# Optimization experiments

Hardware: AMD Instinct MI355X
Metric: run time of the kernel (lower is better)

Reference implementation:

```python
import jax, jax.numpy as jnp
import numpy as np

N = 100000   # nodes
E = 1600000  # edges (avg degree 16)
D = 32       # feature dim

def setup_inputs() -> dict:
    key = jax.random.key(0)
    k1, k2, k3, k4 = jax.random.split(key, 4)
    feat = jax.random.normal(k1, (N, D), dtype=jnp.float32)
    e_feat = jax.random.normal(k2, (E, 1), dtype=jnp.float32)
    src = jax.random.randint(k3, (E,), 0, N)
    dst = jax.random.randint(k4, (E,), 0, N)
    return {"feat": feat, "e_feat": e_feat, "src": src, "dst": dst}

def reference(feat, e_feat, src, dst):
    n = feat.shape[0]
    ones = jnp.ones(src.shape[0], dtype=feat.dtype)
    # degrees computed on the full graph (before self-loop removal), as in DGL code
    out_deg = jax.ops.segment_sum(ones, src, num_segments=n)
    in_deg = jax.ops.segment_sum(ones, dst, num_segments=n)
    src_norm = jnp.power(jnp.clip(out_deg, 1.0, None), -0.5)[:, None]  # [N,1]
    dst_norm = jnp.power(jnp.clip(in_deg, 1.0, None), -0.5)[:, None]   # [N,1]
    # remove_self_loop: mask out self-loop edges in the aggregation only
    mask = (src != dst).astype(feat.dtype)[:, None]                    # [E,1]
    # u_mul_e: gather normalized src features, multiply by edge weight
    msg = (feat * src_norm)[src] * (e_feat * mask)                     # [E,D]
    agg = jax.ops.segment_sum(msg, dst, num_segments=n)                # [N,D]
    out = feat - agg * dst_norm
    return jnp.sum(jnp.abs(out), axis=1)                               # [N]
```

## Files before the change

kernel.cpp:

```cpp
#include <hip/hip_runtime.h>

#define D 32
#define RANGE 128
#define RMAX 800
#define CAP 2304
#define STRIDE 2560
#define SSTRIDE 2560
#define CPAD 16
#define DCH 5000
#define SCH 9000
#define CNT_OFF 50000
#define CUR_OFF 53200
#define ARENA_SZ 56400

__device__ __forceinline__ int scan512(int x, int* wp, int t) {
    int lane = t & 63, w = t >> 6;
    #pragma unroll
    for (int d = 1; d < 64; d <<= 1) {
        int y = __shfl_up(x, d, 64);
        if (lane >= d) x += y;
    }
    if (lane == 63) wp[w] = x;
    __syncthreads();
    int off = 0;
    #pragma unroll
    for (int i = 0; i < 7; i++) if (i < w) off += wp[i];
    return x + off;
}

__global__ __launch_bounds__(256) void zero_cur(int* __restrict__ p, int m) {
    int i = blockIdx.x * 256 + threadIdx.x;
    if (i < m) p[i] = 0;
}

__global__ __launch_bounds__(512) void fused_sort(
        const int* __restrict__ src, const int* __restrict__ dst,
        const float* __restrict__ ef,
        uint2* __restrict__ recsR, unsigned char* __restrict__ srcsR,
        int* __restrict__ gcurD, int* __restrict__ gcurS,
        int E, int DJC) {
    __shared__ __align__(16) char arena[ARENA_SZ];
    __shared__ int wp[8];
    int t = threadIdx.x;
    int* cnt = (int*)(arena + CNT_OFF);
    int* cur = (int*)(arena + CUR_OFF);

    if ((int)blockIdx.x < DJC) {
        int j = blockIdx.x;
        uint2* sd = (uint2*)arena;
        unsigned short* rg16 = (unsigned short*)(arena + 40000);
        int e0 = j * DCH, e1 = min(E, e0 + DCH), cntE = e1 - e0;
        for (int i = t; i < RMAX; i += 512) cnt[i] = 0;
        __syncthreads();
        for (int e = e0 + 2 * t; e < e1; e += 1024) {
            if (e + 1 < e1) {
                int2 d2 = *(const int2*)(dst + e);
                atomicAdd(&cnt[d2.x >> 7], 1);
                atomicAdd(&cnt[d2.y >> 7], 1);
            } else {
                atomicAdd(&cnt[dst[e] >> 7], 1);
            }
        }
        __syncthreads();
        int v0 = cnt[t];
        int incl0 = scan512(v0, wp, t);
        int tot0 = wp[0] + wp[1] + wp[2] + wp[3] + wp[4] + wp[5] + wp[6] + wp[7];
        __syncthreads();
        int i1 = t + 512;
        int v1 = (i1 < RMAX) ? cnt[i1] : 0;
        int incl1 = scan512(v1, wp, t);
        cur[t] = incl0 - v0;
        if (i1 < RMAX) cur[i1] = tot0 + incl1 - v1;
        __syncthreads();
        for (int e = e0 + t; e < e1; e += 512) {
            int s = src[e], d = dst[e];
            float w = (s == d) ? 0.0f : ef[e];
            int rg = d >> 7;
            int pos = atomicAdd(&cur[rg], 1);
            sd[pos] = make_uint2((unsigned)s | ((unsigned)(d & 127) << 17),
                                 __float_as_uint(w));
            rg16[pos] = (unsigned short)rg;
        }
        __syncthreads();
        for (int i = t; i < RMAX; i += 512) {
            int c = cnt[i];
            if (c) {
                int g = atomicAdd(&gcurD[i * CPAD], c);
                cnt[i] = g - (cur[i] - c);
            }
        }
        __syncthreads();
        for (int i = t; i < cntE; i += 512) {
            int rg = rg16[i];
            recsR[(size_t)rg * STRIDE + cnt[rg] + i] = sd[i];
        }
    } else {
        int j = blockIdx.x - DJC;
        unsigned char* sid = (unsigned char*)arena;
        unsigned short* rg16 = (unsigned short*)(arena + 9000);
        int e0 = j * SCH, e1 = min(E, e0 + SCH), cntE = e1 - e0;
        for (int i = t; i < RMAX; i += 512) cnt[i] = 0;
        __syncthreads();
        for (int e = e0 + 2 * t; e < e1; e += 1024) {
            if (e + 1 < e1) {
                int2 s2 = *(const int2*)(src + e);
                atomicAdd(&cnt[s2.x >> 7], 1);
                atomicAdd(&cnt[s2.y >> 7], 1);
            } else {
                atomicAdd(&cnt[src[e] >> 7], 1);
            }
        }
        __syncthreads();
        int v0 = cnt[t];
        int incl0 = scan512(v0, wp, t);
        int tot0 = wp[0] + wp[1] + wp[2] + wp[3] + wp[4] + wp[5] + wp[6] + wp[7];
        __syncthreads();
        int i1 = t + 512;
        int v1 = (i1 < RMAX) ? cnt[i1] : 0;
        int incl1 = scan512(v1, wp, t);
        cur[t] = incl0 - v0;
        if (i1 < RMAX) cur[i1] = tot0 + incl1 - v1;
        __syncthreads();
        for (int e = e0 + t; e < e1; e += 512) {
            int s = src[e];
            int rg = s >> 7;
            int pos = atomicAdd(&cur[rg], 1);
            sid[pos] = (unsigned char)(s & 127);
            rg16[pos] = (unsigned short)rg;
        }
        __syncthreads();
        for (int i = t; i < RMAX; i += 512) {
            int c = cnt[i];
            if (c) {
                int g = atomicAdd(&gcurS[i * CPAD], c);
                cnt[i] = g - (cur[i] - c);
            }
        }
        __syncthreads();
        for (int i = t; i < cntE; i += 512) {
            int rg = rg16[i];
            srcsR[(size_t)rg * SSTRIDE + cnt[rg] + i] = sid[i];
        }
    }
}

__global__ __launch_bounds__(512) void srcnorm_convert(
        const unsigned char* __restrict__ srcsR, const int* __restrict__ gcurS,
        const float* __restrict__ feat, float* __restrict__ featn,
        int n, int R) {
    __shared__ int h[2][RANGE];
    __shared__ int cnt[RANGE];
    int r = blockIdx.x, t = threadIdx.x;
    int base = r * RANGE, lim = min(n - base, RANGE);
    if (t < 256) h[t >> 7][t & 127] = 0;
    __syncthreads();
    int total = gcurS[r * CPAD];
    const unsigned char* p = srcsR + (size_t)r * SSTRIDE;
    int cp = (t >> 8) & 1;
    for (int i = t; i < total; i += 512)
        atomicAdd(&h[cp][p[i]], 1);
    __syncthreads();
    if (t < RANGE) cnt[t] = h[0][t] + h[1][t];
    __syncthreads();
    int total4 = lim * 8;
    for (int i = t; i < total4; i += 512) {
        int row = i >> 3;
        float sn = rsqrtf((float)max(cnt[row], 1));
        float4 f = ((const float4*)(feat + (size_t)(base + row) * D))[i & 7];
        float4 o;
        o.x = f.x * sn; o.y = f.y * sn; o.z = f.z * sn; o.w = f.w * sn;
        ((float4*)(featn + (size_t)(base + row) * D))[i & 7] = o;
    }
}

__global__ __launch_bounds__(512) void gather_kernel(
        const float* __restrict__ feat, const float* __restrict__ featn,
        const uint2* __restrict__ recsR, const int* __restrict__ gcurD,
        float* __restrict__ out, int n, int R) {
    __shared__ uint2 raw[CAP];
    __shared__ uint2 srec[CAP];
    __shared__ int indeg[RANGE];
    __shared__ int pre[RANGE + 1];
    __shared__ int wp[8];
    int r = blockIdx.x, t = threadIdx.x;
    int base = r * RANGE, lim = min(n - base, RANGE);
    int total = gcurD[r * CPAD];
    bool ovf = total > CAP;
    const uint2* reg = recsR + (size_t)r * STRIDE;
    if (t < RANGE) indeg[t] = 0;
    __syncthreads();
    if (!ovf) {
        for (int i = t; i < total; i += 512) {
            uint2 rec = reg[i];
            raw[i] = rec;
            atomicAdd(&indeg[rec.x >> 17], 1);
        }
    } else {
        for (int i = t; i < total; i += 512)
            atomicAdd(&indeg[reg[i].x >> 17], 1);
    }
    __syncthreads();
    int vv = (t < RANGE) ? indeg[t] : 0;
    int incl2 = scan512(vv, wp, t);
    if (t < RANGE) pre[t + 1] = incl2;
    if (t == 0) pre[0] = 0;
    __syncthreads();
    if (t < RANGE) indeg[t] = pre[t];
    __syncthreads();
    if (!ovf) {
        for (int i = t; i < total; i += 512) {
            uint2 rec = raw[i];
            int dl = rec.x >> 17;
            int pos = atomicAdd(&indeg[dl], 1);
            srec[pos] = make_uint2(rec.x & 0x1FFFFu, rec.y);
        }
    }
    __syncthreads();
    int node = t >> 2;
    int cch = t & 3;
    if (node >= lim) return;
    int p0i = pre[node];
    int cnt = pre[node + 1] - p0i;
    float a0 = 0.f, a1 = 0.f, a2 = 0.f, a3 = 0.f, a4 = 0.f, a5 = 0.f, a6 = 0.f, a7 = 0.f;
    if (!ovf) {
        const uint2* sp = srec + p0i;
        int i = 0;
        for (; i + 4 <= cnt; i += 4) {
            uint2 q0 = sp[i], q1 = sp[i + 1], q2 = sp[i + 2], q3 = sp[i + 3];
            const float4* f0 = (const float4*)(featn + (size_t)q0.x * D) + cch * 2;
            const float4* f1 = (const float4*)(featn + (size_t)q1.x * D) + cch * 2;
            const float4* f2 = (const float4*)(featn + (size_t)q2.x * D) + cch * 2;
            const float4* f3 = (const float4*)(featn + (size_t)q3.x * D) + cch * 2;
            float4 A0 = f0[0], B0 = f0[1];
            float4 A1 = f1[0], B1 = f1[1];
            float4 A2 = f2[0], B2 = f2[1];
            float4 A3 = f3[0], B3 = f3[1];
            float w0 = __uint_as_float(q0.y), w1 = __uint_as_float(q1.y);
            float w2 = __uint_as_float(q2.y), w3 = __uint_as_float(q3.y);
            a0 += A0.x * w0 + A1.x * w1 + A2.x * w2 + A3.x * w3;
            a1 += A0.y * w0 + A1.y * w1 + A2.y * w2 + A3.y * w3;
            a2 += A0.z * w0 + A1.z * w1 + A2.z * w2 + A3.z * w3;
            a3 += A0.w * w0 + A1.w * w1 + A2.w * w2 + A3.w * w3;
            a4 += B0.x * w0 + B1.x * w1 + B2.x * w2 + B3.x * w3;
            a5 += B0.y * w0 + B1.y * w1 + B2.y * w2 + B3.y * w3;
            a6 += B0.z * w0 + B1.z * w1 + B2.z * w2 + B3.z * w3;
            a7 += B0.w * w0 + B1.w * w1 + B2.w * w2 + B3.w * w3;
        }
        for (; i < cnt; i++) {
            uint2 q = sp[i];
            const float4* f = (const float4*)(featn + (size_t)q.x * D) + cch * 2;
            float4 A = f[0], B = f[1];
            float w = __uint_as_float(q.y);
            a0 += A.x * w; a1 += A.y * w; a2 += A.z * w; a3 += A.w * w;
            a4 += B.x * w; a5 += B.y * w; a6 += B.z * w; a7 += B.w * w;
        }
    } else {
        for (int k = 0; k < total; k++) {
            uint2 rec = reg[k];
            if ((int)(rec.x >> 17) == node) {
                const float4* f = (const float4*)(featn + (size_t)(rec.x & 0x1FFFFu) * D) + cch * 2;
                float4 A = f[0], B = f[1];
                float w = __uint_as_float(rec.y);
                a0 += A.x * w; a1 += A.y * w; a2 += A.z * w; a3 += A.w * w;
                a4 += B.x * w; a5 += B.y * w; a6 += B.z * w; a7 += B.w * w;
            }
        }
    }
    float dn = rsqrtf((float)max(cnt, 1));
    const float4* fr = (const float4*)(feat + (size_t)(base + node) * D);
    float4 fA = fr[cch * 2];
    float4 fB = fr[cch * 2 + 1];
    float v = fabsf(fA.x - a0 * dn) + fabsf(fA.y - a1 * dn) +
              fabsf(fA.z - a2 * dn) + fabsf(fA.w - a3 * dn) +
              fabsf(fB.x - a4 * dn) + fabsf(fB.y - a5 * dn) +
              fabsf(fB.z - a6 * dn) + fabsf(fB.w - a7 * dn);
    v += __shfl_xor(v, 1, 4);
    v += __shfl_xor(v, 2, 4);
    if (cch == 0) out[base + node] = v;
}

extern "C" void kernel_launch(void* const* d_in, const int* in_sizes, int n_in,
                              void* d_out, int out_size, void* d_ws, size_t ws_size,
                              hipStream_t stream) {
    const float* feat   = (const float*)d_in[0];
    const float* e_feat = (const float*)d_in[1];
    const int*   src    = (const int*)d_in[2];
    const int*   dst    = (const int*)d_in[3];
    const int E = in_sizes[2];
    const int n = in_sizes[0] / D;
    float* out = (float*)d_out;

    const int R   = (n + RANGE - 1) / RANGE;
    const int DJC = (E + DCH - 1) / DCH;
    const int SJC = (E + SCH - 1) / SCH;

    char* p = (char*)d_ws;
    uint2* recsR        = (uint2*)p;         p += ((size_t)R * STRIDE * 8 + 15) & ~(size_t)15;
    unsigned char* srcsR = (unsigned char*)p; p += ((size_t)R * SSTRIDE + 15) & ~(size_t)15;
    int* gcurD          = (int*)p;           p += ((size_t)2 * R * CPAD * 4 + 15) & ~(size_t)15;
    int* gcurS          = gcurD + (size_t)R * CPAD;
    float* featn        = (float*)p;

    const int mcur = R * CPAD * 2;
    zero_cur<<<(mcur + 255) / 256, 256, 0, stream>>>(gcurD, mcur);

    fused_sort<<<DJC + SJC, 512, 0, stream>>>(src, dst, e_feat, recsR, srcsR,
                                              gcurD, gcurS, E, DJC);

    srcnorm_convert<<<R, 512, 0, stream>>>(srcsR, gcurS, feat, featn, n, R);

    gather_kernel<<<R, 512, 0, stream>>>(feat, featn, recsR, gcurD, out, n, R);
}
```

Measured before the change: 140.6 us.

## Fuse sort, source-norm and gather into one cooperative persistent kernel with grid barriers

Replaces the three separate launches (bucket sort, source-degree normalisation with featn materialisation, gather) with one persistent cooperative kernel that loops over work items and separates phases with atomic grid barriers. The source-norm phase now writes only a per-node scale table instead of a scaled copy of the feature matrix. The gather folds that scale into each edge weight and reads raw feat. The raw staging buffer in shared memory is dropped, and chunk sizes are retuned so the grid fits resident blocks. This removes launch gaps and the featn write/read traffic, at the cost of barrier spin overhead, lower occupancy from the larger LDS arena, and a deadlock risk if the fallback non-cooperative launch is ever used.

```diff
diff --git a/kernel.cpp b/kernel.cpp
--- a/kernel.cpp
+++ b/kernel.cpp
@@ -7,11 +7,13 @@
 #define STRIDE 2560
 #define SSTRIDE 2560
 #define CPAD 16
-#define DCH 5000
-#define SCH 9000
-#define CNT_OFF 50000
-#define CUR_OFF 53200
-#define ARENA_SZ 56400
+#define NBLK 512
+#define DCH 5800
+#define RG_OFF 46400
+#define CNT_OFF 58000
+#define CUR_OFF 61200
+#define ARENA_SZ 64400
+#define SRG_OFF 8192
 
 __device__ __forceinline__ int scan512(int x, int* wp, int t) {
     int lane = t & 63, w = t >> 6;
@@ -28,255 +30,254 @@
     return x + off;
 }
 
-__global__ __launch_bounds__(256) void zero_cur(int* __restrict__ p, int m) {
+__global__ __launch_bounds__(256) void zero_ws(int* __restrict__ p, int m) {
     int i = blockIdx.x * 256 + threadIdx.x;
     if (i < m) p[i] = 0;
 }
 
-__global__ __launch_bounds__(512) void fused_sort(
+__device__ __forceinline__ void gridbar(int* c, int target) {
+    __syncthreads();
+    __threadfence();
+    if (threadIdx.x == 0) {
+        atomicAdd(c, 1);
+        while (atomicAdd(c, 0) < target) __builtin_amdgcn_s_sleep(2);
+    }
+    __syncthreads();
+    __threadfence();
+}
+
+__global__ __launch_bounds__(NBLK, 4) void mega(
         const int* __restrict__ src, const int* __restrict__ dst,
-        const float* __restrict__ ef,
+        const float* __restrict__ ef, const float* __restrict__ feat,
         uint2* __restrict__ recsR, unsigned char* __restrict__ srcsR,
-        int* __restrict__ gcurD, int* __restrict__ gcurS,
-        int E, int DJC) {
+        int* __restrict__ gcurD, int* __restrict__ gcurS, int* __restrict__ bars,
+        float* __restrict__ sn_tab, float* __restrict__ out,
+        int n, int R, int E, int DJC, int SCH) {
     __shared__ __align__(16) char arena[ARENA_SZ];
     __shared__ int wp[8];
-    int t = threadIdx.x;
+    int t = threadIdx.x, bid = blockIdx.x, gb = gridDim.x;
     int* cnt = (int*)(arena + CNT_OFF);
     int* cur = (int*)(arena + CUR_OFF);
 
-    if ((int)blockIdx.x < DJC) {
-        int j = blockIdx.x;
-        uint2* sd = (uint2*)arena;
-        unsigned short* rg16 = (unsigned short*)(arena + 40000);
-        int e0 = j * DCH, e1 = min(E, e0 + DCH), cntE = e1 - e0;
-        for (int i = t; i < RMAX; i += 512) cnt[i] = 0;
+    int SJCk = (E + SCH - 1) / SCH;
+    int TC = DJC + SJCk;
+    for (int c = bid; c < TC; c += gb) {
         __syncthreads();
-        for (int e = e0 + 2 * t; e < e1; e += 1024) {
-            if (e + 1 < e1) {
-                int2 d2 = *(const int2*)(dst + e);
-                atomicAdd(&cnt[d2.x >> 7], 1);
-                atomicAdd(&cnt[d2.y >> 7], 1);
-            } else {
-                atomicAdd(&cnt[dst[e] >> 7], 1);
+        if (c < DJC) {
+            uint2* sd = (uint2*)arena;
+            unsigned short* rg16 = (unsigned short*)(arena + RG_OFF);
+            int e0 = c * DCH, e1 = min(E, e0 + DCH), cntE = e1 - e0;
+            for (int i = t; i < RMAX; i += NBLK) cnt[i] = 0;
+            __syncthreads();
+            for (int e = e0 + 2 * t; e < e1; e += 2 * NBLK) {
+                if (e + 1 < e1) {
+                    int2 d2 = *(const int2*)(dst + e);
+                    atomicAdd(&cnt[d2.x >> 7], 1);
+                    atomicAdd(&cnt[d2.y >> 7], 1);
+                } else {
+                    atomicAdd(&cnt[dst[e] >> 7], 1);
+                }
+            }
+            __syncthreads();
+            int v0 = cnt[t];
+            int incl0 = scan512(v0, wp, t);
+            int tot0 = wp[0] + wp[1] + wp[2] + wp[3] + wp[4] + wp[5] + wp[6] + wp[7];
+            __syncthreads();
+            int i1 = t + 512;
+            int v1 = (i1 < RMAX) ? cnt[i1] : 0;
+            int incl1 = scan512(v1, wp, t);
+            cur[t] = incl0 - v0;
+            if (i1 < RMAX) cur[i1] = tot0 + incl1 - v1;
+            __syncthreads();
+            for (int e = e0 + t; e < e1; e += NBLK) {
+                int s = src[e], d = dst[e];
+                float w = (s == d) ? 0.0f : ef[e];
+                int rg = d >> 7;
+                int pos = atomicAdd(&cur[rg], 1);
+                sd[pos] = make_uint2((unsigned)s | ((unsigned)(d & 127) << 17),
+                                     __float_as_uint(w));
+                rg16[pos] = (unsigned short)rg;
+            }
+            __syncthreads();
+            for (int i = t; i < RMAX; i += NBLK) {
+                int cc = cnt[i];
+                if (cc) {
+                    int g = atomicAdd(&gcurD[i * CPAD], cc);
+                    cnt[i] = g - (cur[i] - cc);
+                }
+            }
+            __syncthreads();
+            for (int i = t; i < cntE; i += NBLK) {
+                int rg = rg16[i];
+                recsR[(size_t)rg * STRIDE + cnt[rg] + i] = sd[i];
+            }
+        } else {
+            int j = c - DJC;
+            unsigned char* sid = (unsigned char*)arena;
+            unsigned short* rg16 = (unsigned short*)(arena + SRG_OFF);
+            int e0 = j * SCH, e1 = min(E, e0 + SCH), cntE = e1 - e0;
+            for (int i = t; i < RMAX; i += NBLK) cnt[i] = 0;
+            __syncthreads();
+            for (int e = e0 + 2 * t; e < e1; e += 2 * NBLK) {
+                if (e + 1 < e1) {
+                    int2 s2 = *(const int2*)(src + e);
+                    atomicAdd(&cnt[s2.x >> 7], 1);
+                    atomicAdd(&cnt[s2.y >> 7], 1);
+                } else {
+                    atomicAdd(&cnt[src[e] >> 7], 1);
+                }
+            }
+            __syncthreads();
+            int v0 = cnt[t];
+            int incl0 = scan512(v0, wp, t);
+            int tot0 = wp[0] + wp[1] + wp[2] + wp[3] + wp[4] + wp[5] + wp[6] + wp[7];
+            __syncthreads();
+            int i1 = t + 512;
+            int v1 = (i1 < RMAX) ? cnt[i1] : 0;
+            int incl1 = scan512(v1, wp, t);
+            cur[t] = incl0 - v0;
+            if (i1 < RMAX) cur[i1] = tot0 + incl1 - v1;
+            __syncthreads();
+            for (int e = e0 + t; e < e1; e += NBLK) {
+                int s = src[e];
+                int rg = s >> 7;
+                int pos = atomicAdd(&cur[rg], 1);
+                sid[pos] = (unsigned char)(s & 127);
+                rg16[pos] = (unsigned short)rg;
+            }
+            __syncthreads();
+            for (int i = t; i < RMAX; i += NBLK) {
+                int cc = cnt[i];
+                if (cc) {
+                    int g = atomicAdd(&gcurS[i * CPAD], cc);
+                    cnt[i] = g - (cur[i] - cc);
+                }
+            }
+            __syncthreads();
+            for (int i = t; i < cntE; i += NBLK) {
+                int rg = rg16[i];
+                srcsR[(size_t)rg * SSTRIDE + cnt[rg] + i] = sid[i];
             }
         }
-        __syncthreads();
-        int v0 = cnt[t];
-        int incl0 = scan512(v0, wp, t);
-        int tot0 = wp[0] + wp[1] + wp[2] + wp[3] + wp[4] + wp[5] + wp[6] + wp[7];
-        __syncthreads();
-        int i1 = t + 512;
-        int v1 = (i1 < RMAX) ? cnt[i1] : 0;
-        int incl1 = scan512(v1, wp, t);
-        cur[t] = incl0 - v0;
-        if (i1 < RMAX) cur[i1] = tot0 + incl1 - v1;
-        __syncthreads();
-        for (int e = e0 + t; e < e1; e += 512) {
-            int s = src[e], d = dst[e];
-            float w = (s == d) ? 0.0f : ef[e];
-            int rg = d >> 7;
-            int pos = atomicAdd(&cur[rg], 1);
-            sd[pos] = make_uint2((unsigned)s | ((unsigned)(d & 127) << 17),
-                                 __float_as_uint(w));
-            rg16[pos] = (unsigned short)rg;
+    }
+    gridbar(&bars[0], gb);
+
+    {
+        int* h0 = (int*)arena;
+        int* h1 = (int*)(arena + 512);
+        for (int r = bid; r < R; r += gb) {
+            __syncthreads();
+            if (t < RANGE) { h0[t] = 0; h1[t] = 0; }
+            __syncthreads();
+            int total = gcurS[r * CPAD];
+            const unsigned char* p = srcsR + (size_t)r * SSTRIDE;
+            int* h = (t & 256) ? h1 : h0;
+            for (int i = t; i < total; i += NBLK) atomicAdd(&h[p[i]], 1);
+            __syncthreads();
+            int base = r * RANGE;
+            if (t < RANGE && base + t < n)
+                sn_tab[base + t] = rsqrtf((float)max(h0[t] + h1[t], 1));
         }
-        __syncthreads();
-        for (int i = t; i < RMAX; i += 512) {
-            int c = cnt[i];
-            if (c) {
-                int g = atomicAdd(&gcurD[i * CPAD], c);
-                cnt[i] = g - (cur[i] - c);
+    }
+    gridbar(&bars[1], gb);
+
+    {
+        uint2* srec = (uint2*)arena;
+        int* indeg = (int*)(arena + 18432);
+        int* pre   = (int*)(arena + 18944);
+        for (int r = bid; r < R; r += gb) {
+            __syncthreads();
+            int base = r * RANGE, lim = min(n - base, RANGE);
+            int total = gcurD[r * CPAD];
+            bool ovf = total > CAP;
+            const uint2* reg = recsR + (size_t)r * STRIDE;
+            if (t < RANGE) indeg[t] = 0;
+            __syncthreads();
+            for (int i = t; i < total; i += NBLK)
+                atomicAdd(&indeg[reg[i].x >> 17], 1);
+            __syncthreads();
+            int vv = (t < RANGE) ? indeg[t] : 0;
+            int incl2 = scan512(vv, wp, t);
+            if (t < RANGE) pre[t + 1] = incl2;
+            if (t == 0) pre[0] = 0;
+            __syncthreads();
+            if (t < RANGE) indeg[t] = pre[t];
+            __syncthreads();
+            if (!ovf) {
+                for (int i = t; i < total; i += NBLK) {
+                    uint2 rec = reg[i];
+                    int s = rec.x & 0x1FFFF;
+                    int pos = atomicAdd(&indeg[rec.x >> 17], 1);
+                    float wn = __uint_as_float(rec.y) * sn_tab[s];
+                    srec[pos] = make_uint2((unsigned)s, __float_as_uint(wn));
+                }
+            }
+            __syncthreads();
+            int node = t >> 2, cch = t & 3;
+            if (node < lim) {
+                int p0i = pre[node];
+                int cnt2 = pre[node + 1] - p0i;
+                float a0 = 0.f, a1 = 0.f, a2 = 0.f, a3 = 0.f,
+                      a4 = 0.f, a5 = 0.f, a6 = 0.f, a7 = 0.f;
+                if (!ovf) {
+                    const uint2* sp = srec + p0i;
+                    int i = 0;
+                    for (; i + 4 <= cnt2; i += 4) {
+                        uint2 q0 = sp[i], q1 = sp[i + 1], q2 = sp[i + 2], q3 = sp[i + 3];
+                        const float4* f0 = (const float4*)(feat + (size_t)q0.x * D) + cch * 2;
+                        const float4* f1 = (const float4*)(feat + (size_t)q1.x * D) + cch * 2;
+                        const float4* f2 = (const float4*)(feat + (size_t)q2.x * D) + cch * 2;
+                        const float4* f3 = (const float4*)(feat + (size_t)q3.x * D) + cch * 2;
+                        float4 A0 = f0[0], B0 = f0[1];
+                        float4 A1 = f1[0], B1 = f1[1];
+                        float4 A2 = f2[0], B2 = f2[1];
+                        float4 A3 = f3[0], B3 = f3[1];
+                        float w0 = __uint_as_float(q0.y), w1 = __uint_as_float(q1.y);
+                        float w2 = __uint_as_float(q2.y), w3 = __uint_as_float(q3.y);
+                        a0 += A0.x * w0 + A1.x * w1 + A2.x * w2 + A3.x * w3;
+                        a1 += A0.y * w0 + A1.y * w1 + A2.y * w2 + A3.y * w3;
+                        a2 += A0.z * w0 + A1.z * w1 + A2.z * w2 + A3.z * w3;
+                        a3 += A0.w * w0 + A1.w * w1 + A2.w * w2 + A3.w * w3;
+                        a4 += B0.x * w0 + B1.x * w1 + B2.x * w2 + B3.x * w3;
+                        a5 += B0.y * w0 + B1.y * w1 + B2.y * w2 + B3.y * w3;
+                        a6 += B0.z * w0 + B1.z * w1 + B2.z * w2 + B3.z * w3;
+                        a7 += B0.w * w0 + B1.w * w1 + B2.w * w2 + B3.w * w3;
+                    }
+                    for (; i < cnt2; i++) {
+                        uint2 q = sp[i];
+                        const float4* f = (const float4*)(feat + (size_t)q.x * D) + cch * 2;
+                        float4 A = f[0], B = f[1];
+                        float w = __uint_as_float(q.y);
+                        a0 += A.x * w; a1 += A.y * w; a2 += A.z * w; a3 += A.w * w;
+                        a4 += B.x * w; a5 += B.y * w; a6 += B.z * w; a7 += B.w * w;
+                    }
+                } else {
+                    for (int k = 0; k < total; k++) {
+                        uint2 rec = reg[k];
+                        if ((int)(rec.x >> 17) == node) {
+                            int s = rec.x & 0x1FFFF;
+                            float w = __uint_as_float(rec.y) * sn_tab[s];
+                            const float4* f = (const float4*)(feat + (size_t)s * D) + cch * 2;
+                            float4 A = f[0], B = f[1];
+                            a0 += A.x * w; a1 += A.y * w; a2 += A.z * w; a3 += A.w * w;
+                            a4 += B.x * w; a5 += B.y * w; a6 += B.z * w; a7 += B.w * w;
+                        }
+                    }
+                }
+                float dn = rsqrtf((float)max(cnt2, 1));
+                const float4* fr = (const float4*)(feat + (size_t)(base + node) * D);
+                float4 fA = fr[cch * 2];
+                float4 fB = fr[cch * 2 + 1];
+                float v = fabsf(fA.x - a0 * dn) + fabsf(fA.y - a1 * dn) +
+                          fabsf(fA.z - a2 * dn) + fabsf(fA.w - a3 * dn) +
+                          fabsf(fB.x - a4 * dn) + fabsf(fB.y - a5 * dn) +
+                          fabsf(fB.z - a6 * dn) + fabsf(fB.w - a7 * dn);
+                v += __shfl_xor(v, 1, 4);
+                v += __shfl_xor(v, 2, 4);
+                if (cch == 0) out[base + node] = v;
             }
         }
-        __syncthreads();
-        for (int i = t; i < cntE; i += 512) {
-            int rg = rg16[i];
-            recsR[(size_t)rg * STRIDE + cnt[rg] + i] = sd[i];
-        }
-    } else {
-        int j = blockIdx.x - DJC;
-        unsigned char* sid = (unsigned char*)arena;
-        unsigned short* rg16 = (unsigned short*)(arena + 9000);
-        int e0 = j * SCH, e1 = min(E, e0 + SCH), cntE = e1 - e0;
-        for (int i = t; i < RMAX; i += 512) cnt[i] = 0;
-        __syncthreads();
-        for (int e = e0 + 2 * t; e < e1; e += 1024) {
-            if (e + 1 < e1) {
-                int2 s2 = *(const int2*)(src + e);
-                atomicAdd(&cnt[s2.x >> 7], 1);
-                atomicAdd(&cnt[s2.y >> 7], 1);
-            } else {
-                atomicAdd(&cnt[src[e] >> 7], 1);
-            }
-        }
-        __syncthreads();
-        int v0 = cnt[t];
-        int incl0 = scan512(v0, wp, t);
-        int tot0 = wp[0] + wp[1] + wp[2] + wp[3] + wp[4] + wp[5] + wp[6] + wp[7];
-        __syncthreads();
-        int i1 = t + 512;
-        int v1 = (i1 < RMAX) ? cnt[i1] : 0;
-        int incl1 = scan512(v1, wp, t);
-        cur[t] = incl0 - v0;
-        if (i1 < RMAX) cur[i1] = tot0 + incl1 - v1;
-        __syncthreads();
-        for (int e = e0 + t; e < e1; e += 512) {
-            int s = src[e];
-            int rg = s >> 7;
-            int pos = atomicAdd(&cur[rg], 1);
-            sid[pos] = (unsigned char)(s & 127);
-            rg16[pos] = (unsigned short)rg;
-        }
-        __syncthreads();
-        for (int i = t; i < RMAX; i += 512) {
-            int c = cnt[i];
-            if (c) {
-                int g = atomicAdd(&gcurS[i * CPAD], c);
-                cnt[i] = g - (cur[i] - c);
-            }
-        }
-        __syncthreads();
-        for (int i = t; i < cntE; i += 512) {
-            int rg = rg16[i];
-            srcsR[(size_t)rg * SSTRIDE + cnt[rg] + i] = sid[i];
-        }
-    }
-}
-
-__global__ __launch_bounds__(512) void srcnorm_convert(
-        const unsigned char* __restrict__ srcsR, const int* __restrict__ gcurS,
-        const float* __restrict__ feat, float* __restrict__ featn,
-        int n, int R) {
-    __shared__ int h[2][RANGE];
-    __shared__ int cnt[RANGE];
-    int r = blockIdx.x, t = threadIdx.x;
-    int base = r * RANGE, lim = min(n - base, RANGE);
-    if (t < 256) h[t >> 7][t & 127] = 0;
-    __syncthreads();
-    int total = gcurS[r * CPAD];
-    const unsigned char* p = srcsR + (size_t)r * SSTRIDE;
-    int cp = (t >> 8) & 1;
-    for (int i = t; i < total; i += 512)
-        atomicAdd(&h[cp][p[i]], 1);
-    __syncthreads();
-    if (t < RANGE) cnt[t] = h[0][t] + h[1][t];
-    __syncthreads();
-    int total4 = lim * 8;
-    for (int i = t; i < total4; i += 512) {
-        int row = i >> 3;
-        float sn = rsqrtf((float)max(cnt[row], 1));
-        float4 f = ((const float4*)(feat + (size_t)(base + row) * D))[i & 7];
-        float4 o;
-        o.x = f.x * sn; o.y = f.y * sn; o.z = f.z * sn; o.w = f.w * sn;
-        ((float4*)(featn + (size_t)(base + row) * D))[i & 7] = o;
-    }
-}
-
-__global__ __launch_bounds__(512) void gather_kernel(
-        const float* __restrict__ feat, const float* __restrict__ featn,
-        const uint2* __restrict__ recsR, const int* __restrict__ gcurD,
-        float* __restrict__ out, int n, int R) {
-    __shared__ uint2 raw[CAP];
-    __shared__ uint2 srec[CAP];
-    __shared__ int indeg[RANGE];
-    __shared__ int pre[RANGE + 1];
-    __shared__ int wp[8];
-    int r = blockIdx.x, t = threadIdx.x;
-    int base = r * RANGE, lim = min(n - base, RANGE);
-    int total = gcurD[r * CPAD];
-    bool ovf = total > CAP;
-    const uint2* reg = recsR + (size_t)r * STRIDE;
-    if (t < RANGE) indeg[t] = 0;
-    __syncthreads();
-    if (!ovf) {
-        for (int i = t; i < total; i += 512) {
-            uint2 rec = reg[i];
-            raw[i] = rec;
-            atomicAdd(&indeg[rec.x >> 17], 1);
-        }
-    } else {
-        for (int i = t; i < total; i += 512)
-            atomicAdd(&indeg[reg[i].x >> 17], 1);
-    }
-    __syncthreads();
-    int vv = (t < RANGE) ? indeg[t] : 0;
-    int incl2 = scan512(vv, wp, t);
-    if (t < RANGE) pre[t + 1] = incl2;
-    if (t == 0) pre[0] = 0;
-    __syncthreads();
-    if (t < RANGE) indeg[t] = pre[t];
-    __syncthreads();
-    if (!ovf) {
-        for (int i = t; i < total; i += 512) {
-            uint2 rec = raw[i];
-            int dl = rec.x >> 17;
-            int pos = atomicAdd(&indeg[dl], 1);
-            srec[pos] = make_uint2(rec.x & 0x1FFFFu, rec.y);
-        }
-    }
-    __syncthreads();
-    int node = t >> 2;
-    int cch = t & 3;
-    if (node >= lim) return;
-    int p0i = pre[node];
-    int cnt = pre[node + 1] - p0i;
-    float a0 = 0.f, a1 = 0.f, a2 = 0.f, a3 = 0.f, a4 = 0.f, a5 = 0.f, a6 = 0.f, a7 = 0.f;
-    if (!ovf) {
-        const uint2* sp = srec + p0i;
-        int i = 0;
-        for (; i + 4 <= cnt; i += 4) {
-            uint2 q0 = sp[i], q1 = sp[i + 1], q2 = sp[i + 2], q3 = sp[i + 3];
-            const float4* f0 = (const float4*)(featn + (size_t)q0.x * D) + cch * 2;
-            const float4* f1 = (const float4*)(featn + (size_t)q1.x * D) + cch * 2;
-            const float4* f2 = (const float4*)(featn + (size_t)q2.x * D) + cch * 2;
-            const float4* f3 = (const float4*)(featn + (size_t)q3.x * D) + cch * 2;
-            float4 A0 = f0[0], B0 = f0[1];
-            float4 A1 = f1[0], B1 = f1[1];
-            float4 A2 = f2[0], B2 = f2[1];
-            float4 A3 = f3[0], B3 = f3[1];
-            float w0 = __uint_as_float(q0.y), w1 = __uint_as_float(q1.y);
-            float w2 = __uint_as_float(q2.y), w3 = __uint_as_float(q3.y);
-            a0 += A0.x * w0 + A1.x * w1 + A2.x * w2 + A3.x * w3;
-            a1 += A0.y * w0 + A1.y * w1 + A2.y * w2 + A3.y * w3;
-            a2 += A0.z * w0 + A1.z * w1 + A2.z * w2 + A3.z * w3;
-            a3 += A0.w * w0 + A1.w * w1 + A2.w * w2 + A3.w * w3;
-            a4 += B0.x * w0 + B1.x * w1 + B2.x * w2 + B3.x * w3;
-            a5 += B0.y * w0 + B1.y * w1 + B2.y * w2 + B3.y * w3;
-            a6 += B0.z * w0 + B1.z * w1 + B2.z * w2 + B3.z * w3;
-            a7 += B0.w * w0 + B1.w * w1 + B2.w * w2 + B3.w * w3;
-        }
-        for (; i < cnt; i++) {
-            uint2 q = sp[i];
-            const float4* f = (const float4*)(featn + (size_t)q.x * D) + cch * 2;
-            float4 A = f[0], B = f[1];
-            float w = __uint_as_float(q.y);
-            a0 += A.x * w; a1 += A.y * w; a2 += A.z * w; a3 += A.w * w;
-            a4 += B.x * w; a5 += B.y * w; a6 += B.z * w; a7 += B.w * w;
-        }
-    } else {
-        for (int k = 0; k < total; k++) {
-            uint2 rec = reg[k];
-            if ((int)(rec.x >> 17) == node) {
-                const float4* f = (const float4*)(featn + (size_t)(rec.x & 0x1FFFFu) * D) + cch * 2;
-                float4 A = f[0], B = f[1];
-                float w = __uint_as_float(rec.y);
-                a0 += A.x * w; a1 += A.y * w; a2 += A.z * w; a3 += A.w * w;
-                a4 += B.x * w; a5 += B.y * w; a6 += B.z * w; a7 += B.w * w;
-            }
-        }
-    }
-    float dn = rsqrtf((float)max(cnt, 1));
-    const float4* fr = (const float4*)(feat + (size_t)(base + node) * D);
-    float4 fA = fr[cch * 2];
-    float4 fB = fr[cch * 2 + 1];
-    float v = fabsf(fA.x - a0 * dn) + fabsf(fA.y - a1 * dn) +
-              fabsf(fA.z - a2 * dn) + fabsf(fA.w - a3 * dn) +
-              fabsf(fB.x - a4 * dn) + fabsf(fB.y - a5 * dn) +
-              fabsf(fB.z - a6 * dn) + fabsf(fB.w - a7 * dn);
-    v += __shfl_xor(v, 1, 4);
-    v += __shfl_xor(v, 2, 4);
-    if (cch == 0) out[base + node] = v;
+    }
 }
 
 extern "C" void kernel_launch(void* const* d_in, const int* in_sizes, int n_in,
@@ -292,22 +293,48 @@
 
     const int R   = (n + RANGE - 1) / RANGE;
     const int DJC = (E + DCH - 1) / DCH;
-    const int SJC = (E + SCH - 1) / SCH;
+    const int SJC = NBLK - DJC;
+    const int SCH = (E + SJC - 1) / SJC;
+
+    static int grid = 0;
+    if (grid == 0) {
+        int occ = 0;
+        hipOccupancyMaxActiveBlocksPerMultiprocessor(&occ, mega, NBLK, 0);
+        hipDeviceProp_t prop;
+        int dev = 0;
+        hipGetDevice(&dev);
+        hipGetDeviceProperties(&prop, dev);
+        int g = occ * prop.multiProcessorCount;
+        if (g < 1) g = 256;
+        if (g > NBLK) g = NBLK;
+        grid = g;
+    }
 
     char* p = (char*)d_ws;
-    uint2* recsR        = (uint2*)p;         p += ((size_t)R * STRIDE * 8 + 15) & ~(size_t)15;
+    uint2* recsR         = (uint2*)p;         p += ((size_t)R * STRIDE * 8 + 15) & ~(size_t)15;
     unsigned char* srcsR = (unsigned char*)p; p += ((size_t)R * SSTRIDE + 15) & ~(size_t)15;
-    int* gcurD          = (int*)p;           p += ((size_t)2 * R * CPAD * 4 + 15) & ~(size_t)15;
-    int* gcurS          = gcurD + (size_t)R * CPAD;
-    float* featn        = (float*)p;
-
-    const int mcur = R * CPAD * 2;
-    zero_cur<<<(mcur + 255) / 256, 256, 0, stream>>>(gcurD, mcur);
-
-    fused_sort<<<DJC + SJC, 512, 0, stream>>>(src, dst, e_feat, recsR, srcsR,
-                                              gcurD, gcurS, E, DJC);
-
-    srcnorm_convert<<<R, 512, 0, stream>>>(srcsR, gcurS, feat, featn, n, R);
-
-    gather_kernel<<<R, 512, 0, stream>>>(feat, featn, recsR, gcurD, out, n, R);
-}
+    int* gcurD           = (int*)p;           p += ((size_t)(2 * R * CPAD + 2) * 4 + 15) & ~(size_t)15;
+    int* gcurS           = gcurD + (size_t)R * CPAD;
+    int* bars            = gcurD + (size_t)2 * R * CPAD;
+    float* sn_tab        = (float*)p;
+
+    const int mcur = 2 * R * CPAD + 2;
+    zero_ws<<<(mcur + 255) / 256, 256, 0, stream>>>(gcurD, mcur);
+
+    const int* a_src = src; const int* a_dst = dst;
+    const float* a_ef = e_feat; const float* a_feat = feat;
+    uint2* a_recsR = recsR; unsigned char* a_srcsR = srcsR;
+    int* a_gcurD = gcurD; int* a_gcurS = gcurS; int* a_bars = bars;
+    float* a_sn = sn_tab; float* a_out = out;
+    int a_n = n, a_R = R, a_E = E, a_DJC = DJC, a_SCH = SCH;
+    void* kargs[] = { &a_src, &a_dst, &a_ef, &a_feat, &a_recsR, &a_srcsR,
+                      &a_gcurD, &a_gcurS, &a_bars, &a_sn, &a_out,
+                      &a_n, &a_R, &a_E, &a_DJC, &a_SCH };
+    hipError_t ce = hipLaunchCooperativeKernel(mega, dim3(grid), dim3(NBLK),
+                                               kargs, 0, stream);
+    if (ce != hipSuccess) {
+        mega<<<grid, NBLK, 0, stream>>>(src, dst, e_feat, feat, recsR, srcsR,
+                                        gcurD, gcurS, bars, sn_tab, out,
+                                        n, R, E, DJC, SCH);
+    }
+}
```

After: 349.7 us. +148.7%, slower.
